# Kernel tuning notes

Measured on AMD Instinct MI355X. Metric: run time of the kernel, lower is better.

The kernel has to match this reference:

```python
import jax, jax.numpy as jnp
import numpy as np

# Production-scale dims (see shape_source)
B = 8            # batch size
P = 32768        # points per sample
Q = 2048         # supernodes per sample
N = B * P        # 262144 total points
S = B * Q        # 16384 total supernodes
MAX_DEG = 32
E = S * MAX_DEG  # 524288 edges
IN_DIM = 16
H = 192          # hidden_dim, divisible by ndim=3, per-dim 64 (even) -> no padding
NDIM = 3
MAX_WAVELENGTH = 10000.0


def sincos_embed(pos):
    # ContinuousSincosEmbed: dim split evenly over ndim, sin/cos halves per coord
    dpn = H // NDIM                                                   # 64
    omega = 1.0 / MAX_WAVELENGTH ** (jnp.arange(0, dpn, 2, dtype=jnp.float32) / dpn)  # [dpn/2]
    out = pos[..., None] * omega                                      # [N, ndim, dpn/2]
    emb = jnp.concatenate([jnp.sin(out), jnp.cos(out)], axis=-1)      # [N, ndim, dpn]
    return emb.reshape(pos.shape[0], H)                               # [N, H]


def setup_inputs() -> dict:
    key = jax.random.key(0)
    ks = jax.random.split(key, 8)
    input_feat = jax.random.normal(ks[0], (N, IN_DIM), jnp.float32)
    input_pos = jax.random.uniform(ks[1], (N, NDIM), jnp.float32) * 100.0
    batch_idx = jnp.repeat(jnp.arange(B, dtype=jnp.int32), P)
    # Q supernodes per sample, globally sorted & unique (as from radius_graph filter)
    ar = jnp.arange(S, dtype=jnp.int32)
    supernode_idxs = (ar // Q) * P + (ar % Q)
    # edges: each supernode is dst of MAX_DEG edges; src within same sample
    dst_idx = jnp.repeat(supernode_idxs, MAX_DEG)
    src_idx = (dst_idx // P) * P + jax.random.randint(ks[2], (E,), 0, P, dtype=jnp.int32)
    # params (LinearProjection = affine)
    W_in = jax.random.normal(ks[3], (IN_DIM, H), jnp.float32) / np.sqrt(IN_DIM)
    b_in = jnp.zeros((H,), jnp.float32)
    W1 = jax.random.normal(ks[4], (2 * H, H), jnp.float32) / np.sqrt(2 * H)
    b1 = jnp.zeros((H,), jnp.float32)
    W2 = jax.random.normal(ks[5], (H, H), jnp.float32) / np.sqrt(H)
    b2 = jnp.zeros((H,), jnp.float32)
    return {"input_feat": input_feat, "input_pos": input_pos,
            "supernode_idxs": supernode_idxs, "batch_idx": batch_idx,
            "src_idx": src_idx, "dst_idx": dst_idx,
            "W_in": W_in, "b_in": b_in, "W1": W1, "b1": b1, "W2": W2, "b2": b2}


def reference(input_feat, input_pos, supernode_idxs, batch_idx, src_idx, dst_idx,
              W_in, b_in, W1, b1, W2, b2):
    # x = input_proj(feat) + pos_embed(pos)        [N, H]
    x = input_feat @ W_in + b_in + sincos_embed(input_pos)
    # gather src/dst node features per edge, concat  [E, 2H]
    m = jnp.concatenate([x[src_idx], x[dst_idx]], axis=1)
    # message MLP: Linear -> GELU(exact) -> Linear   [E, H]
    m = jax.nn.gelu(m @ W1 + b1, approximate=False) @ W2 + b2
    # segment-mean by destination supernode (segment_csr 'mean' equivalent)
    seg = jnp.searchsorted(supernode_idxs, dst_idx)  # [E] in [0, S)
    sums = jax.ops.segment_sum(m, seg, num_segments=S)
    cnt = jax.ops.segment_sum(jnp.ones((E,), m.dtype), seg, num_segments=S)
    pooled = sums / cnt[:, None]                     # [S, H]
    return pooled.reshape(B, S // B, H)              # [B, Q, H]
```

## Files before the change

kernel.cpp:

```cpp
#include <hip/hip_runtime.h>
#include <hip/hip_bf16.h>


#define HD 192
#define INF 16
#define N_NODES 262144
#define N_SUP 16384
#define ROWB 384
#define EP_TILES 8

typedef __attribute__((ext_vector_type(8))) short bf16x8;
typedef __attribute__((ext_vector_type(4))) float f32x4;

__device__ __forceinline__ unsigned f2bf(float f) {
    unsigned x = __float_as_uint(f);
    return (x + 0x7fffu + ((x >> 16) & 1u)) >> 16;
}
__device__ __forceinline__ float bf2f(unsigned short u) {
    return __uint_as_float(((unsigned)u) << 16);
}
__device__ __forceinline__ void gload16(const void* g, void* l) {
    __builtin_amdgcn_global_load_lds(
        (const __attribute__((address_space(1))) unsigned int*)g,
        (__attribute__((address_space(3))) unsigned int*)l, 16, 0, 0);
}
__device__ __forceinline__ void gelu_acc(float v, float& acc) {
    const float m   = v * fmaf(v * v, -0.1029392f, -2.3021178f);
    const float den = 1.f + exp2f(m);
    const float r   = __builtin_amdgcn_rcpf(den);
    acc = fmaf(v, r, acc);
}

__global__ void prep_kernel(const float* __restrict__ W1,
                            const float* __restrict__ Win,
                            unsigned short* __restrict__ Wt,
                            unsigned short* __restrict__ Wb,
                            float* __restrict__ Wint)
{
    const int i = blockIdx.x * 256 + threadIdx.x;
    if (i < 36864) {
        const int n = i / HD, k = i % HD;
        Wt[i] = (unsigned short)f2bf(W1[k * HD + n]);
    } else if (i < 73728) {
        const int j = i - 36864;
        const int n = j / HD, k = j % HD;
        Wb[j] = (unsigned short)f2bf(W1[(size_t)(HD + k) * HD + n]);
    } else if (i < 76800) {
        const int j = i - 73728;
        const int c = j / INF, k = j % INF;
        Wint[j] = Win[k * HD + c];
    }
}

__global__ __launch_bounds__(256, 3)
void xcomp_kernel(const float* __restrict__ feat,
                  const float* __restrict__ pos,
                  const float* __restrict__ Wint,
                  const float* __restrict__ bin,
                  unsigned short* __restrict__ xswz)
{
    __shared__ __align__(16) float feat_s[4][256];
    __shared__ float pos_s[4][48];
    __shared__ __align__(16) unsigned short dstg[4][16 * HD];

    const int t = threadIdx.x, w = t >> 6, l = t & 63;

    float win[3][INF];
    #pragma unroll
    for (int d = 0; d < 3; ++d)
        #pragma unroll
        for (int q = 0; q < 4; ++q)
            *reinterpret_cast<float4*>(&win[d][q * 4]) =
                *reinterpret_cast<const float4*>(Wint + (size_t)(l + 64 * d) * INF + q * 4);
    float bcol[3];
    #pragma unroll
    for (int d = 0; d < 3; ++d) bcol[d] = bin[l + 64 * d];
    const float om = exp2f(-(float)(l & 31) * 0.41524101186098287f);
    const float phase = (l < 32) ? 0.f : 1.57079632679f;

    int row0 = blockIdx.x * 256 + w * 16;
    float4 fstage = *reinterpret_cast<const float4*>(
        feat + (size_t)(row0 + (l >> 2)) * INF + (l & 3) * 4);
    float pstage = (l < 48) ? pos[(size_t)row0 * 3 + l] : 0.f;

    for (int gg = 0; gg < 4; ++gg) {
        *reinterpret_cast<float4*>(&feat_s[w][(l >> 2) * 16 + (l & 3) * 4]) = fstage;
        if (l < 48) pos_s[w][l] = pstage;

        const int nrow0 = row0 + 64;
        if (gg < 3) {
            fstage = *reinterpret_cast<const float4*>(
                feat + (size_t)(nrow0 + (l >> 2)) * INF + (l & 3) * 4);
            if (l < 48) pstage = pos[(size_t)nrow0 * 3 + l];
        }

        for (int r = 0; r < 16; ++r) {
            float fr[INF];
            #pragma unroll
            for (int q = 0; q < 4; ++q)
                *reinterpret_cast<float4*>(&fr[q * 4]) =
                    *reinterpret_cast<const float4*>(&feat_s[w][r * 16 + q * 4]);
            #pragma unroll
            for (int d = 0; d < 3; ++d) {
                const float pe = __sinf(fmaf(pos_s[w][r * 3 + d], om, phase));
                float acc = bcol[d] + pe;
                #pragma unroll
                for (int k = 0; k < INF; ++k) acc = fmaf(fr[k], win[d][k], acc);
                dstg[w][r * HD + l + 64 * d] = (unsigned short)f2bf(acc);
            }
        }

        #pragma unroll
        for (int q = 0; q < 6; ++q) {
            const int id = q * 64 + l;
            const int rl = id / 24, c = id % 24;
            const bf16x8 v = *reinterpret_cast<const bf16x8*>(&dstg[w][rl * HD + c * 8]);
            *reinterpret_cast<bf16x8*>((char*)xswz +
                (size_t)(row0 + rl) * ROWB + ((c ^ (rl & 7)) * 16)) = v;
        }
        row0 = nrow0;
    }
}

template<bool GATHER>
__global__ __launch_bounds__(256, 2)
void agemm_kernel(const unsigned short* __restrict__ xswz,
                  const int* __restrict__ gidx,
                  const unsigned short* __restrict__ Wt,
                  const float* __restrict__ bias,
                  unsigned short* __restrict__ outp,
                  const int out_stride,
                  const int ntiles)
{
    __shared__ __align__(16) unsigned short xbuf[2][64 * HD];
    __shared__ int nid[64];

    const int t = threadIdx.x, w = t >> 6, l = t & 63;

    bf16x8 bfr[3][6];
    #pragma unroll
    for (int ct = 0; ct < 3; ++ct) {
        const int col = w * 48 + ct * 16 + (l & 15);
        const unsigned short* wp = Wt + (size_t)col * HD + (l >> 4) * 8;
        #pragma unroll
        for (int ks = 0; ks < 6; ++ks)
            bfr[ct][ks] = *reinterpret_cast<const bf16x8*>(wp + ks * 32);
    }
    float bias_c[3] = {0.f, 0.f, 0.f};
    if (GATHER) {
        #pragma unroll
        for (int ct = 0; ct < 3; ++ct) bias_c[ct] = bias[w * 48 + ct * 16 + (l & 15)];
        if (t < 64) nid[t] = gidx[blockIdx.x * 64 + t];
        __syncthreads();
    }

    auto STAGE = [&](int tile, int buf) {
        char* lbase = (char*)&xbuf[buf][0];
        if constexpr (GATHER) {
            #pragma unroll
            for (int i = 0; i < 6; ++i) {
                const int slot = w * 64 + i * 256 + l;
                const int r = slot / 24, p = slot % 24;
                const int node = nid[r];
                const char* src = (const char*)xswz + (size_t)node * ROWB +
                                  (((p ^ (r & 7)) ^ (node & 7)) * 16);
                gload16(src, lbase + w * 1024 + i * 4096);
            }
        } else {
            const char* gb = (const char*)xswz +
                             (size_t)(blockIdx.x * ntiles + tile) * 64 * ROWB;
            #pragma unroll
            for (int i = 0; i < 6; ++i)
                gload16(gb + w * 1024 + i * 4096 + l * 16, lbase + w * 1024 + i * 4096);
        }
    };

    STAGE(0, 0);
    __syncthreads();

    for (int tt = 0; tt < ntiles; ++tt) {
        const int cur = tt & 1;
        if (tt + 1 < ntiles) STAGE(tt + 1, cur ^ 1);

        f32x4 acc[4][3];
        #pragma unroll
        for (int rt = 0; rt < 4; ++rt)
            #pragma unroll
            for (int ct = 0; ct < 3; ++ct)
                acc[rt][ct] = (f32x4){0.f, 0.f, 0.f, 0.f};

        const char* xb = (const char*)&xbuf[cur][0];
        #pragma unroll
        for (int ks = 0; ks < 6; ++ks) {
            bf16x8 af[4];
            #pragma unroll
            for (int rt = 0; rt < 4; ++rt) {
                const int row = rt * 16 + (l & 15);
                const int p = (ks * 4 + (l >> 4)) ^ (l & 7);
                af[rt] = *reinterpret_cast<const bf16x8*>(xb + row * ROWB + p * 16);
            }
            #pragma unroll
            for (int rt = 0; rt < 4; ++rt)
                #pragma unroll
                for (int ct = 0; ct < 3; ++ct)
                    acc[rt][ct] = __builtin_amdgcn_mfma_f32_16x16x32_bf16(
                        af[rt], bfr[ct][ks], acc[rt][ct], 0, 0, 0);
        }
        __syncthreads();

        char* db = (char*)&xbuf[cur][0];
        #pragma unroll
        for (int rt = 0; rt < 4; ++rt)
            #pragma unroll
            for (int ct = 0; ct < 3; ++ct) {
                const int col = w * 48 + ct * 16 + (l & 15);
                const int ch = col >> 3, off = col & 7;
                #pragma unroll
                for (int j = 0; j < 4; ++j) {
                    const int row = rt * 16 + (l >> 4) * 4 + j;
                    *reinterpret_cast<unsigned short*>(
                        db + row * ROWB + ((ch ^ (row & 7)) * 16) + off * 2) =
                        (unsigned short)f2bf(acc[rt][ct][j] + bias_c[ct]);
                }
            }
        const size_t orow0 = GATHER ? (size_t)blockIdx.x * 64
                                    : (size_t)(blockIdx.x * ntiles + tt) * 64;
        #pragma unroll
        for (int q = 0; q < 6; ++q) {
            const int id = q * 64 + l;
            const int rid = id / 6, cc = id % 6;
            const int c = w * 6 + cc;
            const bf16x8 v = *reinterpret_cast<const bf16x8*>(
                db + rid * ROWB + ((c ^ (rid & 7)) * 16));
            *reinterpret_cast<bf16x8*>(outp + (orow0 + rid) * out_stride + c * 8) = v;
        }
        __syncthreads();
    }
}

__global__ __launch_bounds__(256, 2)
void edgepool_kernel(const unsigned short* __restrict__ xswz,
                     const int* __restrict__ src_idx,
                     const unsigned short* __restrict__ Wt,
                     const unsigned short* __restrict__ bC,
                     float* __restrict__ g)
{
    __shared__ __align__(16) unsigned short xbuf[3][64 * HD];
    __shared__ int sIdx[EP_TILES * 64];
    __shared__ unsigned short bs[EP_TILES * 2 * HD];

    const int t = threadIdx.x, w = t >> 6, l = t & 63;

    #pragma unroll
    for (int i = 0; i < (EP_TILES * 64) / 256; ++i)
        sIdx[t + i * 256] = src_idx[(size_t)blockIdx.x * (EP_TILES * 64) + t + i * 256];
    {
        const size_t srow0 = (size_t)blockIdx.x * (EP_TILES * 2);
        #pragma unroll
        for (int i = 0; i < 6; ++i) {
            const int idx = t + i * 256;
            const int r = idx / 96, c = idx % 96;
            reinterpret_cast<unsigned*>(bs)[idx] =
                *reinterpret_cast<const unsigned*>(bC + (srow0 + r) * 384 + c * 2);
        }
    }

    bf16x8 bfr[3][6];
    #pragma unroll
    for (int ct = 0; ct < 3; ++ct) {
        const int col = w * 48 + ct * 16 + (l & 15);
        const unsigned short* wp = Wt + (size_t)col * HD + (l >> 4) * 8;
        #pragma unroll
        for (int ks = 0; ks < 6; ++ks)
            bfr[ct][ks] = *reinterpret_cast<const bf16x8*>(wp + ks * 32);
    }

    int rr[6], pp[6];
    #pragma unroll
    for (int i = 0; i < 6; ++i) {
        const int slot = w * 64 + i * 256 + l;
        rr[i] = slot / 24; pp[i] = slot % 24;
    }

    __syncthreads();

    auto STAGE = [&](int tile, int buf) {
        char* lbase = (char*)&xbuf[buf][0] + w * 1024;
        const int* se = &sIdx[tile * 64];
        #pragma unroll
        for (int i = 0; i < 6; ++i) {
            const int node = se[rr[i]];
            const char* src = (const char*)xswz + (size_t)node * ROWB +
                              (((pp[i] ^ (rr[i] & 7)) ^ (node & 7)) * 16);
            gload16(src, lbase + i * 4096);
        }
    };

    STAGE(0, 0);
    STAGE(1, 1);

    #pragma unroll 1
    for (int tt = 0; tt < EP_TILES; ++tt) {
        if (tt == 0) { asm volatile("s_waitcnt vmcnt(6)" ::: "memory"); }
        else         { asm volatile("s_waitcnt vmcnt(12)" ::: "memory"); }
        __builtin_amdgcn_s_barrier();
        __builtin_amdgcn_sched_barrier(0);

        if (tt + 2 < EP_TILES) STAGE(tt + 2, (tt + 2) % 3);

        f32x4 acc[4][3];
        #pragma unroll
        for (int rt = 0; rt < 4; ++rt)
            #pragma unroll
            for (int ct = 0; ct < 3; ++ct)
                acc[rt][ct] = (f32x4){0.f, 0.f, 0.f, 0.f};

        const char* xb = (const char*)&xbuf[tt % 3][0];
        #pragma unroll
        for (int ks = 0; ks < 6; ++ks) {
            bf16x8 af[4];
            #pragma unroll
            for (int rt = 0; rt < 4; ++rt) {
                const int row = rt * 16 + (l & 15);
                const int p = (ks * 4 + (l >> 4)) ^ (l & 7);
                af[rt] = *reinterpret_cast<const bf16x8*>(xb + row * ROWB + p * 16);
            }
            #pragma unroll
            for (int rt = 0; rt < 4; ++rt)
                #pragma unroll
                for (int ct = 0; ct < 3; ++ct)
                    acc[rt][ct] = __builtin_amdgcn_mfma_f32_16x16x32_bf16(
                        af[rt], bfr[ct][ks], acc[rt][ct], 0, 0, 0);
        }

        const int s0l = tt * 2;
        #pragma unroll
        for (int sn = 0; sn < 2; ++sn)
            #pragma unroll
            for (int ct = 0; ct < 3; ++ct) {
                const float bval = bf2f(bs[(s0l + sn) * HD + w * 48 + ct * 16 + (l & 15)]);
                float part = 0.f;
                #pragma unroll
                for (int r2 = 0; r2 < 2; ++r2)
                    #pragma unroll
                    for (int j = 0; j < 4; ++j)
                        gelu_acc(acc[sn * 2 + r2][ct][j] + bval, part);
                part += __shfl_xor(part, 16);
                part += __shfl_xor(part, 32);
                if (l < 16)
                    g[((size_t)blockIdx.x * (EP_TILES * 2) + s0l + sn) * HD +
                      w * 48 + ct * 16 + l] = part * 0.03125f;
            }
    }
}

__global__ __launch_bounds__(256, 2)
void gemm192_kernel(const float* __restrict__ A,
                    const float* __restrict__ W,
                    const float* __restrict__ bias,
                    float* __restrict__ out)
{
    __shared__ float xsf[64][196];
    __shared__ float wchunk[32][HD];
    const int t    = threadIdx.x;
    const int row0 = blockIdx.x * 64;

    const float4* ap = reinterpret_cast<const float4*>(A + (size_t)row0 * HD);
    #pragma unroll
    for (int q = 0; q < 12; ++q) {
        const int f4 = t + q * 256;
        const int r = f4 / 48, c = f4 % 48;
        *reinterpret_cast<float4*>(&xsf[r][c * 4]) = ap[f4];
    }

    const int tr = t >> 4;
    const int tc = t & 15;
    float acc[4][12];
    #pragma unroll
    for (int i = 0; i < 4; ++i)
        #pragma unroll
        for (int j = 0; j < 12; ++j) acc[i][j] = 0.f;

    for (int kc = 0; kc < 6; ++kc) {
        __syncthreads();
        {
            const float4* wp = reinterpret_cast<const float4*>(W + kc * 32 * HD);
            float4* wsp = reinterpret_cast<float4*>(&wchunk[0][0]);
            #pragma unroll
            for (int q = 0; q < 6; ++q) wsp[t + q * 256] = wp[t + q * 256];
        }
        __syncthreads();
        #pragma unroll 4
        for (int k = 0; k < 32; ++k) {
            const int kg = kc * 32 + k;
            float xv[4];
            #pragma unroll
            for (int i = 0; i < 4; ++i) xv[i] = xsf[tr * 4 + i][kg];
            float wv[12];
            #pragma unroll
            for (int j4 = 0; j4 < 3; ++j4)
                *reinterpret_cast<float4*>(&wv[j4 * 4]) =
                    *reinterpret_cast<const float4*>(&wchunk[k][tc * 12 + j4 * 4]);
            #pragma unroll
            for (int i = 0; i < 4; ++i)
                #pragma unroll
                for (int j = 0; j < 12; ++j)
                    acc[i][j] = fmaf(xv[i], wv[j], acc[i][j]);
        }
    }

    float bb[12];
    #pragma unroll
    for (int j = 0; j < 12; ++j) bb[j] = bias[tc * 12 + j];

    #pragma unroll
    for (int i = 0; i < 4; ++i) {
        float* o = out + (size_t)(row0 + tr * 4 + i) * HD + tc * 12;
        #pragma unroll
        for (int j4 = 0; j4 < 3; ++j4) {
            float4 v;
            v.x = acc[i][j4 * 4 + 0] + bb[j4 * 4 + 0];
            v.y = acc[i][j4 * 4 + 1] + bb[j4 * 4 + 1];
            v.z = acc[i][j4 * 4 + 2] + bb[j4 * 4 + 2];
            v.w = acc[i][j4 * 4 + 3] + bb[j4 * 4 + 3];
            *reinterpret_cast<float4*>(o + j4 * 4) = v;
        }
    }
}

extern "C" void kernel_launch(void* const* d_in, const int* in_sizes, int n_in,
                              void* d_out, int out_size, void* d_ws, size_t ws_size,
                              hipStream_t stream)
{
    const float* feat = (const float*)d_in[0];
    const float* pos  = (const float*)d_in[1];
    const int*   sup  = (const int*)d_in[2];
    const int*   src  = (const int*)d_in[4];
    const float* Win  = (const float*)d_in[6];
    const float* bin  = (const float*)d_in[7];
    const float* W1   = (const float*)d_in[8];
    const float* b1   = (const float*)d_in[9];
    const float* W2   = (const float*)d_in[10];
    const float* b2   = (const float*)d_in[11];

    char* ws = (char*)d_ws;
    unsigned short* Wt   = (unsigned short*)ws;
    unsigned short* Wb   = (unsigned short*)(ws + 73728);
    float*          Wint = (float*)(ws + 147456);
    unsigned short* x    = (unsigned short*)(ws + 159744);
    char*           C    = ws + 159744 + 100663296;
    float* out = (float*)d_out;

    prep_kernel<<<300, 256, 0, stream>>>(W1, Win, Wt, Wb, Wint);
    xcomp_kernel<<<N_NODES / 256, 256, 0, stream>>>(feat, pos, Wint, bin, x);
    agemm_kernel<true><<<N_SUP / 64, 256, 0, stream>>>(
        x, sup, Wb, b1, (unsigned short*)C, 384, 1);
    edgepool_kernel<<<N_SUP / (2 * EP_TILES), 256, 0, stream>>>(
        x, src, Wt, (const unsigned short*)C, (float*)C);
    gemm192_kernel<<<N_SUP / 64, 256, 0, stream>>>((const float*)C, W2, b2, out);
}
```

Measured before the change: 260.9 us.

## Recompute node embeddings on the fly inside gather GEMM instead of materializing x

```diff
diff --git a/kernel.cpp b/kernel.cpp
--- a/kernel.cpp
+++ b/kernel.cpp
@@ -6,7 +6,6 @@
 #define INF 16
 #define N_NODES 262144
 #define N_SUP 16384
-#define ROWB 384
 #define EP_TILES 8
 
 typedef __attribute__((ext_vector_type(8))) short bf16x8;
@@ -18,11 +17,6 @@
 }
 __device__ __forceinline__ float bf2f(unsigned short u) {
     return __uint_as_float(((unsigned)u) << 16);
-}
-__device__ __forceinline__ void gload16(const void* g, void* l) {
-    __builtin_amdgcn_global_load_lds(
-        (const __attribute__((address_space(1))) unsigned int*)g,
-        (__attribute__((address_space(3))) unsigned int*)l, 16, 0, 0);
 }
 __device__ __forceinline__ void gelu_acc(float v, float& acc) {
     const float m   = v * fmaf(v * v, -0.1029392f, -2.3021178f);
@@ -52,18 +46,24 @@
     }
 }
 
-__global__ __launch_bounds__(256, 3)
-void xcomp_kernel(const float* __restrict__ feat,
+__global__ __launch_bounds__(256, 2)
+void bcomp_kernel(const float* __restrict__ feat,
                   const float* __restrict__ pos,
+                  const int*   __restrict__ sup,
                   const float* __restrict__ Wint,
                   const float* __restrict__ bin,
-                  unsigned short* __restrict__ xswz)
+                  const unsigned short* __restrict__ Wb,
+                  const float* __restrict__ b1,
+                  unsigned short* __restrict__ outp)
 {
+    __shared__ __align__(16) unsigned short xs[2][64 * HD];
     __shared__ __align__(16) float feat_s[4][256];
     __shared__ float pos_s[4][48];
-    __shared__ __align__(16) unsigned short dstg[4][16 * HD];
+    __shared__ int nid[64];
 
     const int t = threadIdx.x, w = t >> 6, l = t & 63;
+
+    if (t < 64) nid[t] = sup[blockIdx.x * 64 + t];
 
     float win[3][INF];
     #pragma unroll
@@ -78,23 +78,176 @@
     const float om = exp2f(-(float)(l & 31) * 0.41524101186098287f);
     const float phase = (l < 32) ? 0.f : 1.57079632679f;
 
-    int row0 = blockIdx.x * 256 + w * 16;
-    float4 fstage = *reinterpret_cast<const float4*>(
-        feat + (size_t)(row0 + (l >> 2)) * INF + (l & 3) * 4);
-    float pstage = (l < 48) ? pos[(size_t)row0 * 3 + l] : 0.f;
-
-    for (int gg = 0; gg < 4; ++gg) {
-        *reinterpret_cast<float4*>(&feat_s[w][(l >> 2) * 16 + (l & 3) * 4]) = fstage;
-        if (l < 48) pos_s[w][l] = pstage;
-
-        const int nrow0 = row0 + 64;
-        if (gg < 3) {
-            fstage = *reinterpret_cast<const float4*>(
-                feat + (size_t)(nrow0 + (l >> 2)) * INF + (l & 3) * 4);
-            if (l < 48) pstage = pos[(size_t)nrow0 * 3 + l];
-        }
-
+    bf16x8 bfr[3][6];
+    #pragma unroll
+    for (int ct = 0; ct < 3; ++ct) {
+        const int col = w * 48 + ct * 16 + (l & 15);
+        const unsigned short* wp = Wb + (size_t)col * HD + (l >> 4) * 8;
+        #pragma unroll
+        for (int ks = 0; ks < 6; ++ks)
+            bfr[ct][ks] = *reinterpret_cast<const bf16x8*>(wp + ks * 32);
+    }
+    float bias_c[3];
+    #pragma unroll
+    for (int ct = 0; ct < 3; ++ct) bias_c[ct] = b1[w * 48 + ct * 16 + (l & 15)];
+
+    __syncthreads();
+
+    {
+        const int nf = nid[w * 16 + (l >> 2)];
+        const float4 fs = *reinterpret_cast<const float4*>(
+            feat + (size_t)nf * INF + (l & 3) * 4);
+        *reinterpret_cast<float4*>(&feat_s[w][(l >> 2) * 16 + (l & 3) * 4]) = fs;
+        if (l < 48) {
+            const int np = nid[w * 16 + l / 3];
+            pos_s[w][l] = pos[(size_t)np * 3 + (l % 3)];
+        }
+    }
+
+    for (int r = 0; r < 16; ++r) {
+        const int n = w * 16 + r;
+        float fr[INF];
+        #pragma unroll
+        for (int q = 0; q < 4; ++q)
+            *reinterpret_cast<float4*>(&fr[q * 4]) =
+                *reinterpret_cast<const float4*>(&feat_s[w][r * 16 + q * 4]);
+        #pragma unroll
+        for (int d = 0; d < 3; ++d) {
+            const float pe = __sinf(fmaf(pos_s[w][r * 3 + d], om, phase));
+            float acc = bcol[d] + pe;
+            #pragma unroll
+            for (int k = 0; k < INF; ++k) acc = fmaf(fr[k], win[d][k], acc);
+            *reinterpret_cast<unsigned short*>(
+                (char*)&xs[0][0] + n * 384 +
+                ((((l >> 3) + 8 * d) ^ (r & 7)) * 16) + (l & 7) * 2) =
+                (unsigned short)f2bf(acc);
+        }
+    }
+    __syncthreads();
+
+    f32x4 acc[4][3];
+    #pragma unroll
+    for (int rt = 0; rt < 4; ++rt)
+        #pragma unroll
+        for (int ct = 0; ct < 3; ++ct)
+            acc[rt][ct] = (f32x4){0.f, 0.f, 0.f, 0.f};
+
+    const char* xb = (const char*)&xs[0][0];
+    #pragma unroll
+    for (int ks = 0; ks < 6; ++ks) {
+        bf16x8 af[4];
+        #pragma unroll
+        for (int rt = 0; rt < 4; ++rt) {
+            const int row = rt * 16 + (l & 15);
+            const int p = (ks * 4 + (l >> 4)) ^ (l & 7);
+            af[rt] = *reinterpret_cast<const bf16x8*>(xb + row * 384 + p * 16);
+        }
+        #pragma unroll
+        for (int rt = 0; rt < 4; ++rt)
+            #pragma unroll
+            for (int ct = 0; ct < 3; ++ct)
+                acc[rt][ct] = __builtin_amdgcn_mfma_f32_16x16x32_bf16(
+                    af[rt], bfr[ct][ks], acc[rt][ct], 0, 0, 0);
+    }
+
+    char* db = (char*)&xs[1][0];
+    #pragma unroll
+    for (int rt = 0; rt < 4; ++rt)
+        #pragma unroll
+        for (int ct = 0; ct < 3; ++ct) {
+            const int col = w * 48 + ct * 16 + (l & 15);
+            const int ch = col >> 3, off = col & 7;
+            #pragma unroll
+            for (int j = 0; j < 4; ++j) {
+                const int row = rt * 16 + (l >> 4) * 4 + j;
+                *reinterpret_cast<unsigned short*>(
+                    db + row * 384 + ((ch ^ (row & 7)) * 16) + off * 2) =
+                    (unsigned short)f2bf(acc[rt][ct][j] + bias_c[ct]);
+            }
+        }
+    __syncthreads();
+    const size_t orow0 = (size_t)blockIdx.x * 64;
+    #pragma unroll
+    for (int q = 0; q < 6; ++q) {
+        const int id = q * 64 + l;
+        const int rid = id / 6, cc = id % 6;
+        const int c = w * 6 + cc;
+        const bf16x8 v = *reinterpret_cast<const bf16x8*>(
+            db + rid * 384 + ((c ^ (rid & 7)) * 16));
+        *reinterpret_cast<bf16x8*>(outp + (orow0 + rid) * 384 + c * 8) = v;
+    }
+}
+
+__global__ __launch_bounds__(256, 2)
+void fusepool_kernel(const float* __restrict__ feat,
+                     const float* __restrict__ pos,
+                     const int* __restrict__ src_idx,
+                     const float* __restrict__ Wint,
+                     const float* __restrict__ bin,
+                     const unsigned short* __restrict__ Wt,
+                     const unsigned short* __restrict__ bC,
+                     float* __restrict__ g)
+{
+    __shared__ __align__(16) unsigned short xs[2][64 * HD];
+    __shared__ __align__(16) float feat_s[4][256];
+    __shared__ float pos_s[4][48];
+    __shared__ int sIdx[EP_TILES * 64];
+    __shared__ unsigned short bs[EP_TILES * 2 * HD];
+
+    const int t = threadIdx.x, w = t >> 6, l = t & 63;
+
+    #pragma unroll
+    for (int i = 0; i < (EP_TILES * 64) / 256; ++i)
+        sIdx[t + i * 256] = src_idx[(size_t)blockIdx.x * (EP_TILES * 64) + t + i * 256];
+    {
+        const size_t srow0 = (size_t)blockIdx.x * (EP_TILES * 2);
+        #pragma unroll
+        for (int i = 0; i < 6; ++i) {
+            const int idx = t + i * 256;
+            const int r = idx / 96, c = idx % 96;
+            reinterpret_cast<unsigned*>(bs)[idx] =
+                *reinterpret_cast<const unsigned*>(bC + (srow0 + r) * 384 + c * 2);
+        }
+    }
+
+    float win[3][INF];
+    #pragma unroll
+    for (int d = 0; d < 3; ++d)
+        #pragma unroll
+        for (int q = 0; q < 4; ++q)
+            *reinterpret_cast<float4*>(&win[d][q * 4]) =
+                *reinterpret_cast<const float4*>(Wint + (size_t)(l + 64 * d) * INF + q * 4);
+    float bcol[3];
+    #pragma unroll
+    for (int d = 0; d < 3; ++d) bcol[d] = bin[l + 64 * d];
+    const float om = exp2f(-(float)(l & 31) * 0.41524101186098287f);
+    const float phase = (l < 32) ? 0.f : 1.57079632679f;
+
+    bf16x8 bfr[3][6];
+    #pragma unroll
+    for (int ct = 0; ct < 3; ++ct) {
+        const int col = w * 48 + ct * 16 + (l & 15);
+        const unsigned short* wp = Wt + (size_t)col * HD + (l >> 4) * 8;
+        #pragma unroll
+        for (int ks = 0; ks < 6; ++ks)
+            bfr[ct][ks] = *reinterpret_cast<const bf16x8*>(wp + ks * 32);
+    }
+
+    __syncthreads();
+
+    auto LOADT = [&](int tile, float4& fs, float& ps) {
+        const int nf = sIdx[tile * 64 + w * 16 + (l >> 2)];
+        fs = *reinterpret_cast<const float4*>(feat + (size_t)nf * INF + (l & 3) * 4);
+        if (l < 48) {
+            const int np = sIdx[tile * 64 + w * 16 + l / 3];
+            ps = pos[(size_t)np * 3 + (l % 3)];
+        }
+    };
+    auto COMPUTE = [&](unsigned short* xbuf, float4 fs, float ps) {
+        *reinterpret_cast<float4*>(&feat_s[w][(l >> 2) * 16 + (l & 3) * 4]) = fs;
+        if (l < 48) pos_s[w][l] = ps;
         for (int r = 0; r < 16; ++r) {
+            const int n = w * 16 + r;
             float fr[INF];
             #pragma unroll
             for (int q = 0; q < 4; ++q)
@@ -106,81 +259,27 @@
                 float acc = bcol[d] + pe;
                 #pragma unroll
                 for (int k = 0; k < INF; ++k) acc = fmaf(fr[k], win[d][k], acc);
-                dstg[w][r * HD + l + 64 * d] = (unsigned short)f2bf(acc);
+                *reinterpret_cast<unsigned short*>(
+                    (char*)xbuf + n * 384 +
+                    ((((l >> 3) + 8 * d) ^ (r & 7)) * 16) + (l & 7) * 2) =
+                    (unsigned short)f2bf(acc);
             }
         }
-
-        #pragma unroll
-        for (int q = 0; q < 6; ++q) {
-            const int id = q * 64 + l;
-            const int rl = id / 24, c = id % 24;
-            const bf16x8 v = *reinterpret_cast<const bf16x8*>(&dstg[w][rl * HD + c * 8]);
-            *reinterpret_cast<bf16x8*>((char*)xswz +
-                (size_t)(row0 + rl) * ROWB + ((c ^ (rl & 7)) * 16)) = v;
-        }
-        row0 = nrow0;
-    }
-}
-
-template<bool GATHER>
-__global__ __launch_bounds__(256, 2)
-void agemm_kernel(const unsigned short* __restrict__ xswz,
-                  const int* __restrict__ gidx,
-                  const unsigned short* __restrict__ Wt,
-                  const float* __restrict__ bias,
-                  unsigned short* __restrict__ outp,
-                  const int out_stride,
-                  const int ntiles)
-{
-    __shared__ __align__(16) unsigned short xbuf[2][64 * HD];
-    __shared__ int nid[64];
-
-    const int t = threadIdx.x, w = t >> 6, l = t & 63;
-
-    bf16x8 bfr[3][6];
-    #pragma unroll
-    for (int ct = 0; ct < 3; ++ct) {
-        const int col = w * 48 + ct * 16 + (l & 15);
-        const unsigned short* wp = Wt + (size_t)col * HD + (l >> 4) * 8;
-        #pragma unroll
-        for (int ks = 0; ks < 6; ++ks)
-            bfr[ct][ks] = *reinterpret_cast<const bf16x8*>(wp + ks * 32);
-    }
-    float bias_c[3] = {0.f, 0.f, 0.f};
-    if (GATHER) {
-        #pragma unroll
-        for (int ct = 0; ct < 3; ++ct) bias_c[ct] = bias[w * 48 + ct * 16 + (l & 15)];
-        if (t < 64) nid[t] = gidx[blockIdx.x * 64 + t];
+    };
+
+    float4 fstage; float pstage = 0.f;
+    LOADT(0, fstage, pstage);
+    COMPUTE(&xs[0][0], fstage, pstage);
+    if (EP_TILES > 1) LOADT(1, fstage, pstage);
+
+    #pragma unroll 1
+    for (int tt = 0; tt < EP_TILES; ++tt) {
         __syncthreads();
-    }
-
-    auto STAGE = [&](int tile, int buf) {
-        char* lbase = (char*)&xbuf[buf][0];
-        if constexpr (GATHER) {
-            #pragma unroll
-            for (int i = 0; i < 6; ++i) {
-                const int slot = w * 64 + i * 256 + l;
-                const int r = slot / 24, p = slot % 24;
-                const int node = nid[r];
-                const char* src = (const char*)xswz + (size_t)node * ROWB +
-                                  (((p ^ (r & 7)) ^ (node & 7)) * 16);
-                gload16(src, lbase + w * 1024 + i * 4096);
-            }
-        } else {
-            const char* gb = (const char*)xswz +
-                             (size_t)(blockIdx.x * ntiles + tile) * 64 * ROWB;
-            #pragma unroll
-            for (int i = 0; i < 6; ++i)
-                gload16(gb + w * 1024 + i * 4096 + l * 16, lbase + w * 1024 + i * 4096);
-        }
-    };
-
-    STAGE(0, 0);
-    __syncthreads();
-
-    for (int tt = 0; tt < ntiles; ++tt) {
-        const int cur = tt & 1;
-        if (tt + 1 < ntiles) STAGE(tt + 1, cur ^ 1);
+
+        if (tt + 1 < EP_TILES) {
+            COMPUTE(&xs[(tt + 1) & 1][0], fstage, pstage);
+            if (tt + 2 < EP_TILES) LOADT(tt + 2, fstage, pstage);
+        }
 
         f32x4 acc[4][3];
         #pragma unroll
@@ -189,7 +288,7 @@
             for (int ct = 0; ct < 3; ++ct)
                 acc[rt][ct] = (f32x4){0.f, 0.f, 0.f, 0.f};
 
-        const char* xb = (const char*)&xbuf[cur][0];
+        const char* xb = (const char*)&xs[tt & 1][0];
         #pragma unroll
         for (int ks = 0; ks < 6; ++ks) {
             bf16x8 af[4];
@@ -197,133 +296,7 @@
             for (int rt = 0; rt < 4; ++rt) {
                 const int row = rt * 16 + (l & 15);
                 const int p = (ks * 4 + (l >> 4)) ^ (l & 7);
-                af[rt] = *reinterpret_cast<const bf16x8*>(xb + row * ROWB + p * 16);
-            }
-            #pragma unroll
-            for (int rt = 0; rt < 4; ++rt)
-                #pragma unroll
-                for (int ct = 0; ct < 3; ++ct)
-                    acc[rt][ct] = __builtin_amdgcn_mfma_f32_16x16x32_bf16(
-                        af[rt], bfr[ct][ks], acc[rt][ct], 0, 0, 0);
-        }
-        __syncthreads();
-
-        char* db = (char*)&xbuf[cur][0];
-        #pragma unroll
-        for (int rt = 0; rt < 4; ++rt)
-            #pragma unroll
-            for (int ct = 0; ct < 3; ++ct) {
-                const int col = w * 48 + ct * 16 + (l & 15);
-                const int ch = col >> 3, off = col & 7;
-                #pragma unroll
-                for (int j = 0; j < 4; ++j) {
-                    const int row = rt * 16 + (l >> 4) * 4 + j;
-                    *reinterpret_cast<unsigned short*>(
-                        db + row * ROWB + ((ch ^ (row & 7)) * 16) + off * 2) =
-                        (unsigned short)f2bf(acc[rt][ct][j] + bias_c[ct]);
-                }
-            }
-        const size_t orow0 = GATHER ? (size_t)blockIdx.x * 64
-                                    : (size_t)(blockIdx.x * ntiles + tt) * 64;
-        #pragma unroll
-        for (int q = 0; q < 6; ++q) {
-            const int id = q * 64 + l;
-            const int rid = id / 6, cc = id % 6;
-            const int c = w * 6 + cc;
-            const bf16x8 v = *reinterpret_cast<const bf16x8*>(
-                db + rid * ROWB + ((c ^ (rid & 7)) * 16));
-            *reinterpret_cast<bf16x8*>(outp + (orow0 + rid) * out_stride + c * 8) = v;
-        }
-        __syncthreads();
-    }
-}
-
-__global__ __launch_bounds__(256, 2)
-void edgepool_kernel(const unsigned short* __restrict__ xswz,
-                     const int* __restrict__ src_idx,
-                     const unsigned short* __restrict__ Wt,
-                     const unsigned short* __restrict__ bC,
-                     float* __restrict__ g)
-{
-    __shared__ __align__(16) unsigned short xbuf[3][64 * HD];
-    __shared__ int sIdx[EP_TILES * 64];
-    __shared__ unsigned short bs[EP_TILES * 2 * HD];
-
-    const int t = threadIdx.x, w = t >> 6, l = t & 63;
-
-    #pragma unroll
-    for (int i = 0; i < (EP_TILES * 64) / 256; ++i)
-        sIdx[t + i * 256] = src_idx[(size_t)blockIdx.x * (EP_TILES * 64) + t + i * 256];
-    {
-        const size_t srow0 = (size_t)blockIdx.x * (EP_TILES * 2);
-        #pragma unroll
-        for (int i = 0; i < 6; ++i) {
-            const int idx = t + i * 256;
-            const int r = idx / 96, c = idx % 96;
-            reinterpret_cast<unsigned*>(bs)[idx] =
-                *reinterpret_cast<const unsigned*>(bC + (srow0 + r) * 384 + c * 2);
-        }
-    }
-
-    bf16x8 bfr[3][6];
-    #pragma unroll
-    for (int ct = 0; ct < 3; ++ct) {
-        const int col = w * 48 + ct * 16 + (l & 15);
-        const unsigned short* wp = Wt + (size_t)col * HD + (l >> 4) * 8;
-        #pragma unroll
-        for (int ks = 0; ks < 6; ++ks)
-            bfr[ct][ks] = *reinterpret_cast<const bf16x8*>(wp + ks * 32);
-    }
-
-    int rr[6], pp[6];
-    #pragma unroll
-    for (int i = 0; i < 6; ++i) {
-        const int slot = w * 64 + i * 256 + l;
-        rr[i] = slot / 24; pp[i] = slot % 24;
-    }
-
-    __syncthreads();
-
-    auto STAGE = [&](int tile, int buf) {
-        char* lbase = (char*)&xbuf[buf][0] + w * 1024;
-        const int* se = &sIdx[tile * 64];
-        #pragma unroll
-        for (int i = 0; i < 6; ++i) {
-            const int node = se[rr[i]];
-            const char* src = (const char*)xswz + (size_t)node * ROWB +
-                              (((pp[i] ^ (rr[i] & 7)) ^ (node & 7)) * 16);
-            gload16(src, lbase + i * 4096);
-        }
-    };
-
-    STAGE(0, 0);
-    STAGE(1, 1);
-
-    #pragma unroll 1
-    for (int tt = 0; tt < EP_TILES; ++tt) {
-        if (tt == 0) { asm volatile("s_waitcnt vmcnt(6)" ::: "memory"); }
-        else         { asm volatile("s_waitcnt vmcnt(12)" ::: "memory"); }
-        __builtin_amdgcn_s_barrier();
-        __builtin_amdgcn_sched_barrier(0);
-
-        if (tt + 2 < EP_TILES) STAGE(tt + 2, (tt + 2) % 3);
-
-        f32x4 acc[4][3];
-        #pragma unroll
-        for (int rt = 0; rt < 4; ++rt)
-            #pragma unroll
-            for (int ct = 0; ct < 3; ++ct)
-                acc[rt][ct] = (f32x4){0.f, 0.f, 0.f, 0.f};
-
-        const char* xb = (const char*)&xbuf[tt % 3][0];
-        #pragma unroll
-        for (int ks = 0; ks < 6; ++ks) {
-            bf16x8 af[4];
-            #pragma unroll
-            for (int rt = 0; rt < 4; ++rt) {
-                const int row = rt * 16 + (l & 15);
-                const int p = (ks * 4 + (l >> 4)) ^ (l & 7);
-                af[rt] = *reinterpret_cast<const bf16x8*>(xb + row * ROWB + p * 16);
+                af[rt] = *reinterpret_cast<const bf16x8*>(xb + row * 384 + p * 16);
             }
             #pragma unroll
             for (int rt = 0; rt < 4; ++rt)
@@ -447,15 +420,13 @@
     unsigned short* Wt   = (unsigned short*)ws;
     unsigned short* Wb   = (unsigned short*)(ws + 73728);
     float*          Wint = (float*)(ws + 147456);
-    unsigned short* x    = (unsigned short*)(ws + 159744);
-    char*           C    = ws + 159744 + 100663296;
+    char*           C    = ws + 159744;
     float* out = (float*)d_out;
 
     prep_kernel<<<300, 256, 0, stream>>>(W1, Win, Wt, Wb, Wint);
-    xcomp_kernel<<<N_NODES / 256, 256, 0, stream>>>(feat, pos, Wint, bin, x);
-    agemm_kernel<true><<<N_SUP / 64, 256, 0, stream>>>(
-        x, sup, Wb, b1, (unsigned short*)C, 384, 1);
-    edgepool_kernel<<<N_SUP / (2 * EP_TILES), 256, 0, stream>>>(
-        x, src, Wt, (const unsigned short*)C, (float*)C);
+    bcomp_kernel<<<N_SUP / 64, 256, 0, stream>>>(
+        feat, pos, sup, Wint, bin, Wb, b1, (unsigned short*)C);
+    fusepool_kernel<<<N_SUP / (2 * EP_TILES), 256, 0, stream>>>(
+        feat, pos, src, Wint, bin, Wt, (const unsigned short*)C, (float*)C);
     gemm192_kernel<<<N_SUP / 64, 256, 0, stream>>>((const float*)C, W2, b2, out);
 }
```

Result: no change. 257.3 us (-1.4%).
